# Optimization experiments

Measured on AMD Instinct MI355X. Metric: run time of the kernel, lower is better.

Reference implementation:

```python
import jax, jax.numpy as jnp
import numpy as np


def _block(x, W, b, use_relu):
    # x: (B, n, dx). Faithful to PairwiseInteractions: full pairwise L2 dist,
    # top-k (k == n) smallest sorted, drop self, concat(self, neighbor), linear,
    # optional relu, mean over the n-1 neighbors.
    B, n, dx = x.shape
    sq = jnp.sum(x * x, axis=-1)                                   # (B, n)
    d2 = sq[:, :, None] + sq[:, None, :] - 2.0 * jnp.einsum('bnd,bmd->bnm', x, x)
    dist = jnp.sqrt(jnp.maximum(d2, 0.0))                          # (B, n, n)
    _, idx = jax.lax.top_k(-dist, n)                               # ascending distances
    idx_nb = idx[:, :, 1:]                                         # drop self -> (B, n, n-1)
    nbr = jnp.take_along_axis(x[:, None, :, :], idx_nb[..., None], axis=2)  # (B, n, n-1, dx)
    self_rep = jnp.broadcast_to(x[:, :, None, :], nbr.shape)
    pairs = jnp.concatenate([self_rep, nbr], axis=-1)              # (B, n, n-1, 2*dx)
    h = pairs @ W + b
    if use_relu:
        h = jax.nn.relu(h)
    return jnp.sum(h, axis=2) / (n - 1)                            # (B, n, d_out)


def setup_inputs() -> dict:
    key = jax.random.key(0)
    ks = jax.random.split(key, 4)
    B, N, d = 2, 1024, 3

    def lin(k, fin, fout):
        kw, kb = jax.random.split(k)
        lim = 1.0 / np.sqrt(fin).astype(np.float32)
        W = jax.random.uniform(kw, (fin, fout), minval=-lim, maxval=lim, dtype=jnp.float32)
        b = jax.random.uniform(kb, (fout,), minval=-lim, maxval=lim, dtype=jnp.float32)
        return W, b

    W1, b1 = lin(ks[1], 2 * d, 32)
    W2, b2 = lin(ks[2], 2 * 32, 64)
    W3, b3 = lin(ks[3], 2 * 64, d)
    x = jax.random.normal(ks[0], (B, N * d), dtype=jnp.float32)
    return {"x": x, "W1": W1, "b1": b1, "W2": W2, "b2": b2, "W3": W3, "b3": b3}


def reference(x, W1, b1, W2, b2, W3, b3):
    B = x.shape[0]
    d = W3.shape[1]
    N = x.shape[1] // d
    h = x.reshape(B, N, d)
    h = _block(h, W1, b1, True)    # eb1: d -> 32, relu
    h = _block(h, W2, b2, True)    # eb2: 32 -> 64, relu
    h = _block(h, W3, b3, False)   # eb3: 64 -> d, no relu
    return h.reshape(B, N * d)
```

## Files before the change

kernel.cpp:

```cpp
#include <hip/hip_runtime.h>

#define NN 1024

__global__ __launch_bounds__(256) void k1_pair32_ac2(
    const float* __restrict__ x,  const float* __restrict__ W1, const float* __restrict__ b1,
    const float* __restrict__ W2, const float* __restrict__ b2,
    float* __restrict__ a2g, float* __restrict__ c2g)
{
    __shared__ float cbuf[8192];
    __shared__ float rowbuf[4][32];

    const int tid  = threadIdx.x;
    const int wave = tid >> 6, lane = tid & 63;
    const int blk  = blockIdx.x;

    const int i  = blk * 4 + wave;
    const int b  = i >> 10;
    const int il = i & 1023;
    const int js = lane >> 5, f = lane & 31;
    const float* xb = x + b * (NN * 3);

    const float xi0 = xb[il*3+0], xi1 = xb[il*3+1], xi2 = xb[il*3+2];
    const float a     = xi0*W1[0*32+f] + xi1*W1[1*32+f] + xi2*W1[2*32+f];
    const float cself = xi0*W1[3*32+f] + xi1*W1[4*32+f] + xi2*W1[5*32+f] + b1[f];

    float acc = 0.f;
    const int f2 = tid & 31, r0 = tid >> 5;
    const float w3f = W1[3*32+f2], w4f = W1[4*32+f2], w5f = W1[5*32+f2], bf = b1[f2];
    for (int tile = 0; tile < NN; tile += 256) {
        #pragma unroll 4
        for (int k = 0; k < 32; ++k) {
            int r = tile + r0 + k*8;
            float y0 = xb[r*3+0], y1 = xb[r*3+1], y2 = xb[r*3+2];
            cbuf[(r0 + k*8)*32 + f2] = y0*w3f + y1*w4f + y2*w5f + bf;
        }
        __syncthreads();
        #pragma unroll 8
        for (int jj = js; jj < 256; jj += 2)
            acc += fmaxf(a + cbuf[jj*32 + f], 0.f);
        __syncthreads();
    }
    acc += __shfl_xor(acc, 32);
    float res = (acc - fmaxf(a + cself, 0.f)) * (1.0f/1023.0f);
    if (js == 0) rowbuf[wave][f] = res;
    __syncthreads();

    float av = 0.f, cv = b2[lane];
    #pragma unroll
    for (int d = 0; d < 32; ++d) {
        float hv = rowbuf[wave][d];
        av += hv * W2[d*64 + lane];
        cv += hv * W2[(32 + d)*64 + lane];
    }
    a2g[i*64 + lane] = av;
    c2g[i*64 + lane] = cv;
}

__global__ __launch_bounds__(256) void k2_pair64_final(
    const float* __restrict__ a2g, const float* __restrict__ c2g,
    const float* __restrict__ W3, const float* __restrict__ b3,
    float* __restrict__ out, float* __restrict__ partials)
{
    __shared__ float cbuf[8192];
    __shared__ float pacc[4][2][64];
    __shared__ float qpart[4][3];

    const int tid  = threadIdx.x;
    const int wave = tid >> 6, lane = tid & 63;
    const int blk  = blockIdx.x;

    const int i0 = blk * 4;
    const int b  = blk >> 8;
    const int rw = wave >> 1, jh = wave & 1;
    const int rowA = i0 + 2*rw, rowB = rowA + 1;

    const float* cb = c2g + b * (NN * 64);
    const float a0 = a2g[rowA*64 + lane];
    const float a1 = a2g[rowB*64 + lane];
    float acc0 = 0.f, acc1 = 0.f;

    for (int tile = 0; tile < NN; tile += 128) {
        const float4* src = (const float4*)(cb + tile * 64);
        float4* dst = (float4*)cbuf;
        for (int k = tid; k < 2048; k += 256) dst[k] = src[k];
        __syncthreads();
        #pragma unroll 8
        for (int k = 0; k < 64; ++k) {
            float c = cbuf[(2*k + jh)*64 + lane];
            acc0 += fmaxf(a0 + c, 0.f);
            acc1 += fmaxf(a1 + c, 0.f);
        }
        __syncthreads();
    }
    pacc[wave][0][lane] = acc0;
    pacc[wave][1][lane] = acc1;
    __syncthreads();

    const int i = i0 + wave;
    const int wpair = 2*(wave >> 1);
    float accf = pacc[wpair][wave & 1][lane] + pacc[wpair + 1][wave & 1][lane];
    float aself = a2g[i*64 + lane];
    float self  = fmaxf(aself + cb[(i & 1023)*64 + lane], 0.f);
    float res = (accf - self) * (1.0f/1023.0f);

    float wt0 = W3[lane*3+0], wt1 = W3[lane*3+1], wt2 = W3[lane*3+2];
    float wb0 = W3[(64+lane)*3+0], wb1 = W3[(64+lane)*3+1], wb2 = W3[(64+lane)*3+2];
    float y0 = res * (wt0 - wb0*(1.0f/1023.0f));
    float y1 = res * (wt1 - wb1*(1.0f/1023.0f));
    float y2 = res * (wt2 - wb2*(1.0f/1023.0f));
    float q0 = res * wb0, q1 = res * wb1, q2 = res * wb2;
    #pragma unroll
    for (int off = 32; off; off >>= 1) {
        y0 += __shfl_xor(y0, off);  y1 += __shfl_xor(y1, off);  y2 += __shfl_xor(y2, off);
        q0 += __shfl_xor(q0, off);  q1 += __shfl_xor(q1, off);  q2 += __shfl_xor(q2, off);
    }
    if (lane == 0) {
        out[i*3+0] = y0 + b3[0];
        out[i*3+1] = y1 + b3[1];
        out[i*3+2] = y2 + b3[2];
        qpart[wave][0] = q0;  qpart[wave][1] = q1;  qpart[wave][2] = q2;
    }
    __syncthreads();
    if (tid < 3)
        partials[blk*3 + tid] = qpart[0][tid] + qpart[1][tid] + qpart[2][tid] + qpart[3][tid];
}

__global__ __launch_bounds__(256) void k3_final(
    const float* __restrict__ partials, float* __restrict__ out)
{
    __shared__ float red[4][3];

    const int tid  = threadIdx.x;
    const int wave = tid >> 6, lane = tid & 63;
    const int blk  = blockIdx.x;
    const int b = blk >> 2;

    const float* pb = partials + b * 256 * 3;
    float s0 = pb[tid*3+0], s1 = pb[tid*3+1], s2 = pb[tid*3+2];
    #pragma unroll
    for (int off = 32; off; off >>= 1) {
        s0 += __shfl_xor(s0, off);  s1 += __shfl_xor(s1, off);  s2 += __shfl_xor(s2, off);
    }
    if (lane == 0) { red[wave][0] = s0; red[wave][1] = s1; red[wave][2] = s2; }
    __syncthreads();
    float S0 = (red[0][0]+red[1][0]+red[2][0]+red[3][0]) * (1.0f/1023.0f);
    float S1 = (red[0][1]+red[1][1]+red[2][1]+red[3][1]) * (1.0f/1023.0f);
    float S2 = (red[0][2]+red[1][2]+red[2][2]+red[3][2]) * (1.0f/1023.0f);

    const int i = b * NN + (blk & 3) * 256 + tid;
    out[i*3+0] += S0;
    out[i*3+1] += S1;
    out[i*3+2] += S2;
}

extern "C" void kernel_launch(void* const* d_in, const int* in_sizes, int n_in,
                              void* d_out, int out_size, void* d_ws, size_t ws_size,
                              hipStream_t stream) {
    const float* x  = (const float*)d_in[0];
    const float* W1 = (const float*)d_in[1];
    const float* b1 = (const float*)d_in[2];
    const float* W2 = (const float*)d_in[3];
    const float* b2 = (const float*)d_in[4];
    const float* W3 = (const float*)d_in[5];
    const float* b3 = (const float*)d_in[6];
    float* out = (float*)d_out;

    float* ws = (float*)d_ws;
    float* a2g      = ws;
    float* c2g      = a2g + 2048*64;
    float* partials = c2g + 2048*64;

    k1_pair32_ac2<<<512, 256, 0, stream>>>(x, W1, b1, W2, b2, a2g, c2g);
    k2_pair64_final<<<512, 256, 0, stream>>>(a2g, c2g, W3, b3, out, partials);
    k3_final<<<8, 256, 0, stream>>>(partials, out);
}
```

Before: 105.3 us.

## Fuse final reduction into k2 via last-block counter, vectorize and prefetch tiles

Removes the third kernel launch by having the last finishing block of k2 (detected with an atomic counter reset in k1) reduce the partials and add the broadcast term to the output. k1 now stages x in shared memory and processes two features per lane with float2 vectors. k2 handles eight rows per block with float2 math and register-prefetches the next c2 tile while computing the current one. This trades launch overhead and global reloads for more registers and halves k2's grid to 256 blocks, which may reduce occupancy.

```diff
diff --git a/kernel.cpp b/kernel.cpp
--- a/kernel.cpp
+++ b/kernel.cpp
@@ -1,48 +1,73 @@
 #include <hip/hip_runtime.h>
+
+typedef float float2v __attribute__((ext_vector_type(2)));
+typedef float float4v __attribute__((ext_vector_type(4)));
 
 #define NN 1024
 
 __global__ __launch_bounds__(256) void k1_pair32_ac2(
     const float* __restrict__ x,  const float* __restrict__ W1, const float* __restrict__ b1,
     const float* __restrict__ W2, const float* __restrict__ b2,
-    float* __restrict__ a2g, float* __restrict__ c2g)
+    float* __restrict__ a2g, float* __restrict__ c2g, unsigned int* __restrict__ counter)
 {
+    __shared__ float xbuf[3072];
     __shared__ float cbuf[8192];
     __shared__ float rowbuf[4][32];
 
     const int tid  = threadIdx.x;
     const int wave = tid >> 6, lane = tid & 63;
     const int blk  = blockIdx.x;
+    if (blk == 0 && tid == 0) *counter = 0u;
 
     const int i  = blk * 4 + wave;
     const int b  = i >> 10;
     const int il = i & 1023;
-    const int js = lane >> 5, f = lane & 31;
-    const float* xb = x + b * (NN * 3);
-
-    const float xi0 = xb[il*3+0], xi1 = xb[il*3+1], xi2 = xb[il*3+2];
-    const float a     = xi0*W1[0*32+f] + xi1*W1[1*32+f] + xi2*W1[2*32+f];
-    const float cself = xi0*W1[3*32+f] + xi1*W1[4*32+f] + xi2*W1[5*32+f] + b1[f];
-
-    float acc = 0.f;
-    const int f2 = tid & 31, r0 = tid >> 5;
-    const float w3f = W1[3*32+f2], w4f = W1[4*32+f2], w5f = W1[5*32+f2], bf = b1[f2];
+    const int js = lane >> 4;
+    const int fp = lane & 15;
+
+    const float4v* xb4 = (const float4v*)(x + b * 3072);
+    {
+        float4v* xd = (float4v*)xbuf;
+        #pragma unroll
+        for (int n = 0; n < 3; ++n) xd[tid + n * 256] = xb4[tid + n * 256];
+    }
+    __syncthreads();
+
+    const float xi0 = xbuf[il*3+0], xi1 = xbuf[il*3+1], xi2 = xbuf[il*3+2];
+    const float2v* W1v = (const float2v*)W1;
+    const float2v* b1v = (const float2v*)b1;
+    float2v a  = xi0*W1v[0*16+fp] + xi1*W1v[1*16+fp] + xi2*W1v[2*16+fp];
+    float2v cs = xi0*W1v[3*16+fp] + xi1*W1v[4*16+fp] + xi2*W1v[5*16+fp] + b1v[fp];
+
+    const int fp2 = tid & 15, r0 = tid >> 4;
+    const float2v w3 = W1v[3*16+fp2], w4 = W1v[4*16+fp2], w5 = W1v[5*16+fp2];
+    const float2v bb = b1v[fp2];
+
+    float2v acc = (float2v)0.f;
+    float2v* cb2w = (float2v*)cbuf;
+    const float2v* cb2 = (const float2v*)cbuf;
     for (int tile = 0; tile < NN; tile += 256) {
-        #pragma unroll 4
-        for (int k = 0; k < 32; ++k) {
-            int r = tile + r0 + k*8;
-            float y0 = xb[r*3+0], y1 = xb[r*3+1], y2 = xb[r*3+2];
-            cbuf[(r0 + k*8)*32 + f2] = y0*w3f + y1*w4f + y2*w5f + bf;
+        #pragma unroll
+        for (int k = 0; k < 16; ++k) {
+            int r = r0 + k * 16;
+            int g = tile + r;
+            float y0 = xbuf[g*3+0], y1 = xbuf[g*3+1], y2 = xbuf[g*3+2];
+            cb2w[r*16 + fp2] = y0*w3 + y1*w4 + y2*w5 + bb;
         }
         __syncthreads();
         #pragma unroll 8
-        for (int jj = js; jj < 256; jj += 2)
-            acc += fmaxf(a + cbuf[jj*32 + f], 0.f);
-        __syncthreads();
-    }
-    acc += __shfl_xor(acc, 32);
-    float res = (acc - fmaxf(a + cself, 0.f)) * (1.0f/1023.0f);
-    if (js == 0) rowbuf[wave][f] = res;
+        for (int k = 0; k < 64; ++k) {
+            float2v c = cb2[(4*k + js)*16 + fp];
+            acc += __builtin_elementwise_max(a + c, (float2v)0.f);
+        }
+        __syncthreads();
+    }
+    acc.x += __shfl_xor(acc.x, 16);  acc.y += __shfl_xor(acc.y, 16);
+    acc.x += __shfl_xor(acc.x, 32);  acc.y += __shfl_xor(acc.y, 32);
+
+    float2v self = __builtin_elementwise_max(a + cs, (float2v)0.f);
+    float2v res  = (acc - self) * (1.0f/1023.0f);
+    if (js == 0) ((float2v*)rowbuf[wave])[fp] = res;
     __syncthreads();
 
     float av = 0.f, cv = b2[lane];
@@ -59,98 +84,134 @@
 __global__ __launch_bounds__(256) void k2_pair64_final(
     const float* __restrict__ a2g, const float* __restrict__ c2g,
     const float* __restrict__ W3, const float* __restrict__ b3,
-    float* __restrict__ out, float* __restrict__ partials)
+    float* __restrict__ out, float* __restrict__ partials, unsigned int* __restrict__ counter)
 {
     __shared__ float cbuf[8192];
-    __shared__ float pacc[4][2][64];
     __shared__ float qpart[4][3];
+    __shared__ float red[4][3];
+    __shared__ unsigned int sLast;
 
     const int tid  = threadIdx.x;
     const int wave = tid >> 6, lane = tid & 63;
     const int blk  = blockIdx.x;
 
-    const int i0 = blk * 4;
-    const int b  = blk >> 8;
-    const int rw = wave >> 1, jh = wave & 1;
-    const int rowA = i0 + 2*rw, rowB = rowA + 1;
+    const int i0 = blk * 8;
+    const int b  = blk >> 7;
+    const int jh = lane >> 5, fp = lane & 31;
+    const int rA = i0 + 2*wave, rB = rA + 1;
 
     const float* cb = c2g + b * (NN * 64);
-    const float a0 = a2g[rowA*64 + lane];
-    const float a1 = a2g[rowB*64 + lane];
-    float acc0 = 0.f, acc1 = 0.f;
-
+    const float2v* a2v = (const float2v*)a2g;
+    const float2v aA = a2v[rA*32 + fp];
+    const float2v aB = a2v[rB*32 + fp];
+    float2v acc0 = (float2v)0.f, acc1 = (float2v)0.f;
+
+    const float4v* src = (const float4v*)cb;
+    float4v regs[8];
+    #pragma unroll
+    for (int n = 0; n < 8; ++n) regs[n] = src[tid + n*256];
+    {
+        float4v* dst = (float4v*)cbuf;
+        #pragma unroll
+        for (int n = 0; n < 8; ++n) dst[tid + n*256] = regs[n];
+    }
+    __syncthreads();
+
+    const float2v* cb2 = (const float2v*)cbuf;
     for (int tile = 0; tile < NN; tile += 128) {
-        const float4* src = (const float4*)(cb + tile * 64);
-        float4* dst = (float4*)cbuf;
-        for (int k = tid; k < 2048; k += 256) dst[k] = src[k];
-        __syncthreads();
+        const bool more = (tile + 128) < NN;
+        if (more) {
+            const float4v* s2 = src + (tile + 128) * 16;
+            #pragma unroll
+            for (int n = 0; n < 8; ++n) regs[n] = s2[tid + n*256];
+        }
         #pragma unroll 8
         for (int k = 0; k < 64; ++k) {
-            float c = cbuf[(2*k + jh)*64 + lane];
-            acc0 += fmaxf(a0 + c, 0.f);
-            acc1 += fmaxf(a1 + c, 0.f);
-        }
-        __syncthreads();
-    }
-    pacc[wave][0][lane] = acc0;
-    pacc[wave][1][lane] = acc1;
-    __syncthreads();
-
-    const int i = i0 + wave;
-    const int wpair = 2*(wave >> 1);
-    float accf = pacc[wpair][wave & 1][lane] + pacc[wpair + 1][wave & 1][lane];
-    float aself = a2g[i*64 + lane];
-    float self  = fmaxf(aself + cb[(i & 1023)*64 + lane], 0.f);
-    float res = (accf - self) * (1.0f/1023.0f);
-
-    float wt0 = W3[lane*3+0], wt1 = W3[lane*3+1], wt2 = W3[lane*3+2];
-    float wb0 = W3[(64+lane)*3+0], wb1 = W3[(64+lane)*3+1], wb2 = W3[(64+lane)*3+2];
-    float y0 = res * (wt0 - wb0*(1.0f/1023.0f));
-    float y1 = res * (wt1 - wb1*(1.0f/1023.0f));
-    float y2 = res * (wt2 - wb2*(1.0f/1023.0f));
-    float q0 = res * wb0, q1 = res * wb1, q2 = res * wb2;
-    #pragma unroll
-    for (int off = 32; off; off >>= 1) {
-        y0 += __shfl_xor(y0, off);  y1 += __shfl_xor(y1, off);  y2 += __shfl_xor(y2, off);
-        q0 += __shfl_xor(q0, off);  q1 += __shfl_xor(q1, off);  q2 += __shfl_xor(q2, off);
+            float2v c = cb2[(2*k + jh)*32 + fp];
+            acc0 += __builtin_elementwise_max(aA + c, (float2v)0.f);
+            acc1 += __builtin_elementwise_max(aB + c, (float2v)0.f);
+        }
+        __syncthreads();
+        if (more) {
+            float4v* dst = (float4v*)cbuf;
+            #pragma unroll
+            for (int n = 0; n < 8; ++n) dst[tid + n*256] = regs[n];
+        }
+        __syncthreads();
+    }
+    acc0.x += __shfl_xor(acc0.x, 32);  acc0.y += __shfl_xor(acc0.y, 32);
+    acc1.x += __shfl_xor(acc1.x, 32);  acc1.y += __shfl_xor(acc1.y, 32);
+
+    const float2v* cbv = (const float2v*)cb;
+    const float inv = 1.0f/1023.0f;
+    float2v res0 = (acc0 - __builtin_elementwise_max(aA + cbv[(rA & 1023)*32 + fp], (float2v)0.f)) * inv;
+    float2v res1 = (acc1 - __builtin_elementwise_max(aB + cbv[(rB & 1023)*32 + fp], (float2v)0.f)) * inv;
+
+    float yA[3], qA[3], yB[3], qB[3];
+    #pragma unroll
+    for (int t = 0; t < 3; ++t) {
+        float wt0 = W3[(2*fp)*3 + t],   wb0 = W3[(64 + 2*fp)*3 + t];
+        float wt1 = W3[(2*fp+1)*3 + t], wb1 = W3[(64 + 2*fp+1)*3 + t];
+        float k0 = wt0 - wb0*inv, k1 = wt1 - wb1*inv;
+        yA[t] = res0.x*k0 + res0.y*k1;   qA[t] = res0.x*wb0 + res0.y*wb1;
+        yB[t] = res1.x*k0 + res1.y*k1;   qB[t] = res1.x*wb0 + res1.y*wb1;
+    }
+    #pragma unroll
+    for (int off = 1; off < 32; off <<= 1) {
+        #pragma unroll
+        for (int t = 0; t < 3; ++t) {
+            yA[t] += __shfl_xor(yA[t], off);  qA[t] += __shfl_xor(qA[t], off);
+            yB[t] += __shfl_xor(yB[t], off);  qB[t] += __shfl_xor(qB[t], off);
+        }
     }
     if (lane == 0) {
-        out[i*3+0] = y0 + b3[0];
-        out[i*3+1] = y1 + b3[1];
-        out[i*3+2] = y2 + b3[2];
-        qpart[wave][0] = q0;  qpart[wave][1] = q1;  qpart[wave][2] = q2;
+        out[rA*3+0] = yA[0] + b3[0];  out[rA*3+1] = yA[1] + b3[1];  out[rA*3+2] = yA[2] + b3[2];
+        out[rB*3+0] = yB[0] + b3[0];  out[rB*3+1] = yB[1] + b3[1];  out[rB*3+2] = yB[2] + b3[2];
+        qpart[wave][0] = qA[0] + qB[0];
+        qpart[wave][1] = qA[1] + qB[1];
+        qpart[wave][2] = qA[2] + qB[2];
     }
     __syncthreads();
     if (tid < 3)
         partials[blk*3 + tid] = qpart[0][tid] + qpart[1][tid] + qpart[2][tid] + qpart[3][tid];
-}
-
-__global__ __launch_bounds__(256) void k3_final(
-    const float* __restrict__ partials, float* __restrict__ out)
-{
-    __shared__ float red[4][3];
-
-    const int tid  = threadIdx.x;
-    const int wave = tid >> 6, lane = tid & 63;
-    const int blk  = blockIdx.x;
-    const int b = blk >> 2;
-
-    const float* pb = partials + b * 256 * 3;
-    float s0 = pb[tid*3+0], s1 = pb[tid*3+1], s2 = pb[tid*3+2];
-    #pragma unroll
-    for (int off = 32; off; off >>= 1) {
-        s0 += __shfl_xor(s0, off);  s1 += __shfl_xor(s1, off);  s2 += __shfl_xor(s2, off);
-    }
-    if (lane == 0) { red[wave][0] = s0; red[wave][1] = s1; red[wave][2] = s2; }
-    __syncthreads();
-    float S0 = (red[0][0]+red[1][0]+red[2][0]+red[3][0]) * (1.0f/1023.0f);
-    float S1 = (red[0][1]+red[1][1]+red[2][1]+red[3][1]) * (1.0f/1023.0f);
-    float S2 = (red[0][2]+red[1][2]+red[2][2]+red[3][2]) * (1.0f/1023.0f);
-
-    const int i = b * NN + (blk & 3) * 256 + tid;
-    out[i*3+0] += S0;
-    out[i*3+1] += S1;
-    out[i*3+2] += S2;
+
+    __threadfence();
+    __syncthreads();
+    if (tid == 0) sLast = (atomicAdd(counter, 1u) == 255u) ? 1u : 0u;
+    __syncthreads();
+    if (!sLast) return;
+    __threadfence();
+
+    {
+        const int half = tid >> 7, kk = tid & 127;
+        const float* pp = partials + (half*128 + kk) * 3;
+        float p0 = pp[0], p1 = pp[1], p2 = pp[2];
+        #pragma unroll
+        for (int off = 1; off < 64; off <<= 1) {
+            p0 += __shfl_xor(p0, off);  p1 += __shfl_xor(p1, off);  p2 += __shfl_xor(p2, off);
+        }
+        if (lane == 0) { red[wave][0] = p0; red[wave][1] = p1; red[wave][2] = p2; }
+    }
+    __syncthreads();
+    float S[2][3];
+    #pragma unroll
+    for (int t = 0; t < 3; ++t) {
+        S[0][t] = (red[0][t] + red[1][t]) * inv;
+        S[1][t] = (red[2][t] + red[3][t]) * inv;
+    }
+    float4v addv[2][3];
+    #pragma unroll
+    for (int bb = 0; bb < 2; ++bb) {
+        addv[bb][0] = (float4v){S[bb][0], S[bb][1], S[bb][2], S[bb][0]};
+        addv[bb][1] = (float4v){S[bb][1], S[bb][2], S[bb][0], S[bb][1]};
+        addv[bb][2] = (float4v){S[bb][2], S[bb][0], S[bb][1], S[bb][2]};
+    }
+    float4v* o4 = (float4v*)out;
+    #pragma unroll
+    for (int n = 0; n < 6; ++n) {
+        int idx = tid + n * 256;
+        o4[idx] += addv[idx >> 9 ? (idx / 768) : 0][idx % 3];
+    }
 }
 
 extern "C" void kernel_launch(void* const* d_in, const int* in_sizes, int n_in,
@@ -166,11 +227,11 @@
     float* out = (float*)d_out;
 
     float* ws = (float*)d_ws;
-    float* a2g      = ws;
-    float* c2g      = a2g + 2048*64;
-    float* partials = c2g + 2048*64;
-
-    k1_pair32_ac2<<<512, 256, 0, stream>>>(x, W1, b1, W2, b2, a2g, c2g);
-    k2_pair64_final<<<512, 256, 0, stream>>>(a2g, c2g, W3, b3, out, partials);
-    k3_final<<<8, 256, 0, stream>>>(partials, out);
+    float* a2g        = ws;
+    float* c2g        = a2g + 131072;
+    float* partials   = c2g + 131072;
+    unsigned int* cnt = (unsigned int*)(partials + 768);
+
+    k1_pair32_ac2<<<512, 256, 0, stream>>>(x, W1, b1, W2, b2, a2g, c2g, cnt);
+    k2_pair64_final<<<256, 256, 0, stream>>>(a2g, c2g, W3, b3, out, partials, cnt);
 }
```

Result: slower. 112.6 us (+7.0%).
